# Kernel optimization log

Measured on AMD Instinct MI355X. Metric: run time of the kernel, lower is better.

Reference implementation:

```python
import jax, jax.numpy as jnp
import numpy as np

N_NODES = 100000
N_EDGES = 1600000
IN_CH = 48
OUT_CH = 64
K = 2


def setup_inputs() -> dict:
    key = jax.random.key(0)
    k1, k2, k3, k4 = jax.random.split(key, 4)
    x = jax.random.normal(k1, (N_NODES, IN_CH), dtype=jnp.float32)
    edge_index = jax.random.randint(k2, (2, N_EDGES), 0, N_NODES, dtype=jnp.int64)
    W = jax.random.normal(k3, (IN_CH, OUT_CH), dtype=jnp.float32) * (1.0 / np.sqrt(IN_CH))
    b = jax.random.normal(k4, (OUT_CH,), dtype=jnp.float32) * 0.01
    return {"x": x, "edge_index": edge_index, "W": W, "b": b}


def _propagate(x, row, col):
    n = x.shape[0]
    # degree of each node counted over col (destination) indices
    deg = jax.ops.segment_sum(jnp.ones_like(col, dtype=x.dtype), col, num_segments=n)
    deg_inv_sqrt = jnp.where(deg > 0, jax.lax.rsqrt(jnp.where(deg > 0, deg, 1.0)), 0.0)
    norm = deg_inv_sqrt[row] * deg_inv_sqrt[col]  # [E]
    # gather-scale-scatter: out[col] += x[row] * norm
    msgs = x[row] * norm[:, None]  # [E, d]
    return jax.ops.segment_sum(msgs, col, num_segments=n)


def reference(x, edge_index, W, b):
    row, col = edge_index[0], edge_index[1]
    h = x
    for _ in range(K):
        h = _propagate(h, row, col)
    return h @ W + b
```

## Files before the change

kernel.cpp:

```cpp
#include <hip/hip_runtime.h>
#include <hip/hip_bf16.h>
#include <hip/hip_fp16.h>


#define N_NODES 100000
#define N_EDGES 1600000
#define IN_CH 48
#define OUT_CH 64
#define NBINS 64
#define NBUCKETS 1024
#define EPB 8192
#define NBLK_EDGE 196

__global__ void bucket_hist_kernel(const int* __restrict__ col, int* __restrict__ bucketCount) {
    __shared__ int lh[NBUCKETS];
    for (int i = threadIdx.x; i < NBUCKETS; i += 256) lh[i] = 0;
    __syncthreads();
    int base = blockIdx.x * EPB;
    #pragma unroll 4
    for (int k = 0; k < 32; k++) {
        int e = base + k * 256 + threadIdx.x;
        if (e < N_EDGES) atomicAdd(&lh[col[e] >> 7], 1);
    }
    __syncthreads();
    for (int i = threadIdx.x; i < NBUCKETS; i += 256)
        if (lh[i]) atomicAdd(&bucketCount[i], lh[i]);
}

__global__ void bucket_scan_kernel(const int* __restrict__ bucketCount,
                                   int* __restrict__ bucketStart,
                                   int* __restrict__ bucketCursor) {
    __shared__ int l[NBUCKETS + 1];
    for (int i = threadIdx.x; i < NBUCKETS; i += 256) l[i] = bucketCount[i];
    __syncthreads();
    if (threadIdx.x == 0) {
        int t = 0;
        for (int k = 0; k < NBUCKETS; k++) { int c = l[k]; l[k] = t; t += c; }
        l[NBUCKETS] = t;
    }
    __syncthreads();
    for (int i = threadIdx.x; i <= NBUCKETS; i += 256) {
        bucketStart[i] = l[i];
        if (i < NBUCKETS) bucketCursor[i] = l[i];
    }
}

__global__ void bucket_scatter_kernel(const int* __restrict__ row, const int* __restrict__ col,
                                      int* __restrict__ bucketCursor, int* __restrict__ bucketed) {
    __shared__ int lh[NBUCKETS];
    __shared__ int lofs[NBUCKETS];
    __shared__ int lbase[NBUCKETS];
    __shared__ int stage[EPB];
    __shared__ unsigned short sbkt[EPB];
    __shared__ int wsum[4];
    int tid = threadIdx.x;
    int base = blockIdx.x * EPB;
    for (int i = tid; i < NBUCKETS; i += 256) lh[i] = 0;
    __syncthreads();
    #pragma unroll 4
    for (int k = 0; k < 32; k++) {
        int e = base + k * 256 + tid;
        if (e < N_EDGES) atomicAdd(&lh[col[e] >> 7], 1);
    }
    __syncthreads();
    int c0 = lh[4 * tid], c1 = lh[4 * tid + 1], c2 = lh[4 * tid + 2], c3 = lh[4 * tid + 3];
    {
        int s = c0 + c1 + c2 + c3;
        int incl = s;
        int lane = tid & 63, w = tid >> 6;
        #pragma unroll
        for (int o = 1; o < 64; o <<= 1) {
            int v = __shfl_up(incl, o, 64);
            if (lane >= o) incl += v;
        }
        if (lane == 63) wsum[w] = incl;
        __syncthreads();
        int wbase = 0;
        for (int k = 0; k < w; k++) wbase += wsum[k];
        int ex = wbase + incl - s;
        lofs[4 * tid]     = ex;
        lofs[4 * tid + 1] = ex + c0;
        lofs[4 * tid + 2] = ex + c0 + c1;
        lofs[4 * tid + 3] = ex + c0 + c1 + c2;
    }
    __syncthreads();
    for (int i = tid; i < NBUCKETS; i += 256) {
        int c = lh[i];
        if (c > 0) lbase[i] = atomicAdd(&bucketCursor[i], c);
        lh[i] = 0;
    }
    __syncthreads();
    #pragma unroll 4
    for (int k = 0; k < 32; k++) {
        int e = base + k * 256 + tid;
        if (e < N_EDGES) {
            int c = col[e];
            int bkt = c >> 7;
            int r = atomicAdd(&lh[bkt], 1);
            int slot = lofs[bkt] + r;
            stage[slot] = (row[e] << 7) | (c & 127);
            sbkt[slot] = (unsigned short)bkt;
        }
    }
    __syncthreads();
    int total = (base + EPB <= N_EDGES) ? EPB : (N_EDGES - base);
    for (int i = tid; i < total; i += 256) {
        int bkt = sbkt[i];
        bucketed[lbase[bkt] + (i - lofs[bkt])] = stage[i];
    }
}

__global__ void fine_sort_kernel(const int* __restrict__ bucketed,
                                 const int* __restrict__ bucketStart,
                                 int* __restrict__ edge_src,
                                 int* __restrict__ deg, int* __restrict__ start,
                                 float* __restrict__ dis, int* __restrict__ binTotal) {
    __shared__ int fh[128];
    __shared__ int sfh[129];
    __shared__ int cur[128];
    __shared__ int bh[NBINS];
    int b = blockIdx.x;
    int s0 = bucketStart[b], s1 = bucketStart[b + 1];
    if (threadIdx.x < 128) fh[threadIdx.x] = 0;
    if (threadIdx.x < NBINS) bh[threadIdx.x] = 0;
    __syncthreads();
    for (int j = s0 + threadIdx.x; j < s1; j += 256)
        atomicAdd(&fh[bucketed[j] & 127], 1);
    __syncthreads();
    if (threadIdx.x == 0) {
        int t = 0;
        for (int k = 0; k < 128; k++) { sfh[k] = t; t += fh[k]; }
        sfh[128] = t;
    }
    __syncthreads();
    if (threadIdx.x < 128) {
        cur[threadIdx.x] = sfh[threadIdx.x];
        int node = b * 128 + threadIdx.x;
        if (node < N_NODES) {
            int d = fh[threadIdx.x];
            deg[node] = d;
            start[node] = s0 + sfh[threadIdx.x];
            dis[node] = (d > 0) ? rsqrtf((float)d) : 0.0f;
            atomicAdd(&bh[min(d, NBINS - 1)], 1);
        }
    }
    __syncthreads();
    for (int j = s0 + threadIdx.x; j < s1; j += 256) {
        int rc = bucketed[j];
        int p = atomicAdd(&cur[rc & 127], 1);
        edge_src[s0 + p] = rc >> 7;
    }
    __syncthreads();
    if (threadIdx.x < NBINS && bh[threadIdx.x])
        atomicAdd(&binTotal[threadIdx.x], bh[threadIdx.x]);
}

__global__ void binscan_kernel(const int* __restrict__ binTotal, int* __restrict__ binCursor) {
    if (threadIdx.x == 0) {
        int t = 0;
        for (int k = NBINS - 1; k >= 0; k--) { binCursor[k] = t; t += binTotal[k]; }
    }
}

__global__ void order_kernel(const int* __restrict__ deg, const int* __restrict__ start,
                             const float* __restrict__ dis, int* __restrict__ binCursor,
                             int4* __restrict__ nodeinfo, int n) {
    __shared__ int lhist[NBINS];
    __shared__ int lbase[NBINS];
    int i = blockIdx.x * 256 + threadIdx.x;
    if (threadIdx.x < NBINS) lhist[threadIdx.x] = 0;
    __syncthreads();
    int bin = 0, myrank = 0;
    if (i < n) {
        bin = min(deg[i], NBINS - 1);
        myrank = atomicAdd(&lhist[bin], 1);
    }
    __syncthreads();
    if (threadIdx.x < NBINS && lhist[threadIdx.x] > 0)
        lbase[threadIdx.x] = atomicAdd(&binCursor[threadIdx.x], lhist[threadIdx.x]);
    __syncthreads();
    if (i < n) {
        int pos = lbase[bin] + myrank;
        nodeinfo[pos] = make_int4(i, start[i], deg[i], __float_as_int(dis[i]));
    }
}

__global__ void prescale_kernel(const float* __restrict__ x, const float* __restrict__ dis,
                                __half2* __restrict__ xs, int n2) {
    int i = blockIdx.x * 256 + threadIdx.x;
    if (i < n2) {
        int node = i / 24;
        float2 v = ((const float2*)x)[i];
        float d = dis[node];
        xs[i] = __floats2half2_rn(v.x * d, v.y * d);
    }
}

#define LOAD3(p, v0, v1, v2) { v0 = (p)[0]; v1 = (p)[1]; v2 = (p)[2]; }
#define ACC6(v0, v1, v2) { \
    float2 u0 = __half22float2(v0), u1 = __half22float2(v1), u2 = __half22float2(v2); \
    a0 += u0.x; a1 += u0.y; a2 += u1.x; a3 += u1.y; a4 += u2.x; a5 += u2.y; }

__global__ void gather1_kernel(const __half2* __restrict__ xs,
                               const int* __restrict__ edge_src,
                               const int4* __restrict__ nodeinfo,
                               __half2* __restrict__ h1) {
    int g = blockIdx.x * 32 + (threadIdx.x >> 3);
    int lane = threadIdx.x & 7;
    int4 ni = nodeinfo[g];
    int node = ni.x, s = ni.y, e = ni.y + ni.z;
    float dv = __int_as_float(ni.w);
    float a0 = 0, a1 = 0, a2 = 0, a3 = 0, a4 = 0, a5 = 0;
    int j = s;
    for (; j + 3 < e; j += 4) {
        int s0 = edge_src[j], s1 = edge_src[j + 1], s2 = edge_src[j + 2], s3 = edge_src[j + 3];
        const __half2* p0 = xs + s0 * 24 + lane * 3;
        const __half2* p1 = xs + s1 * 24 + lane * 3;
        const __half2* p2 = xs + s2 * 24 + lane * 3;
        const __half2* p3 = xs + s3 * 24 + lane * 3;
        __half2 v00, v01, v02, v10, v11, v12, v20, v21, v22, v30, v31, v32;
        LOAD3(p0, v00, v01, v02);
        LOAD3(p1, v10, v11, v12);
        LOAD3(p2, v20, v21, v22);
        LOAD3(p3, v30, v31, v32);
        ACC6(v00, v01, v02);
        ACC6(v10, v11, v12);
        ACC6(v20, v21, v22);
        ACC6(v30, v31, v32);
    }
    for (; j < e; ++j) {
        const __half2* p0 = xs + edge_src[j] * 24 + lane * 3;
        __half2 v00, v01, v02;
        LOAD3(p0, v00, v01, v02);
        ACC6(v00, v01, v02);
    }
    float sc = dv * dv;
    __half2* q = h1 + node * 24 + lane * 3;
    q[0] = __floats2half2_rn(a0 * sc, a1 * sc);
    q[1] = __floats2half2_rn(a2 * sc, a3 * sc);
    q[2] = __floats2half2_rn(a4 * sc, a5 * sc);
}

__global__ void gather2_gemm_kernel(const __half2* __restrict__ h1,
                                    const int* __restrict__ edge_src,
                                    const int4* __restrict__ nodeinfo,
                                    const float* __restrict__ W,
                                    const float* __restrict__ b,
                                    float* __restrict__ out) {
    __shared__ float sW[IN_CH * OUT_CH];
    __shared__ float sb[OUT_CH];
    __shared__ float sh[32][IN_CH + 1];

    for (int i = threadIdx.x; i < IN_CH * OUT_CH; i += 256) sW[i] = W[i];
    if (threadIdx.x < OUT_CH) sb[threadIdx.x] = b[threadIdx.x];

    int nl = threadIdx.x >> 3;
    int lane = threadIdx.x & 7;
    int g = blockIdx.x * 32 + nl;
    int4 ni = nodeinfo[g];
    int node = ni.x, s = ni.y, e = ni.y + ni.z;
    float dv = __int_as_float(ni.w);

    float a0 = 0, a1 = 0, a2 = 0, a3 = 0, a4 = 0, a5 = 0;
    int j = s;
    for (; j + 3 < e; j += 4) {
        int s0 = edge_src[j], s1 = edge_src[j + 1], s2 = edge_src[j + 2], s3 = edge_src[j + 3];
        const __half2* p0 = h1 + s0 * 24 + lane * 3;
        const __half2* p1 = h1 + s1 * 24 + lane * 3;
        const __half2* p2 = h1 + s2 * 24 + lane * 3;
        const __half2* p3 = h1 + s3 * 24 + lane * 3;
        __half2 v00, v01, v02, v10, v11, v12, v20, v21, v22, v30, v31, v32;
        LOAD3(p0, v00, v01, v02);
        LOAD3(p1, v10, v11, v12);
        LOAD3(p2, v20, v21, v22);
        LOAD3(p3, v30, v31, v32);
        ACC6(v00, v01, v02);
        ACC6(v10, v11, v12);
        ACC6(v20, v21, v22);
        ACC6(v30, v31, v32);
    }
    for (; j < e; ++j) {
        const __half2* p0 = h1 + edge_src[j] * 24 + lane * 3;
        __half2 v00, v01, v02;
        LOAD3(p0, v00, v01, v02);
        ACC6(v00, v01, v02);
    }
    int c0 = 6 * lane;
    sh[nl][c0 + 0] = a0 * dv;
    sh[nl][c0 + 1] = a1 * dv;
    sh[nl][c0 + 2] = a2 * dv;
    sh[nl][c0 + 3] = a3 * dv;
    sh[nl][c0 + 4] = a4 * dv;
    sh[nl][c0 + 5] = a5 * dv;
    __syncthreads();

    int j0 = lane * 8;
    float acc[8];
    #pragma unroll
    for (int i = 0; i < 8; i++) acc[i] = sb[j0 + i];
    for (int k = 0; k < IN_CH; k++) {
        float s0 = sh[nl][k];
        #pragma unroll
        for (int i = 0; i < 8; i++) acc[i] += s0 * sW[k * OUT_CH + j0 + i];
    }
    float4* o = (float4*)(out + (size_t)node * OUT_CH + j0);
    o[0] = make_float4(acc[0], acc[1], acc[2], acc[3]);
    o[1] = make_float4(acc[4], acc[5], acc[6], acc[7]);
}

extern "C" void kernel_launch(void* const* d_in, const int* in_sizes, int n_in,
                              void* d_out, int out_size, void* d_ws, size_t ws_size,
                              hipStream_t stream) {
    const float* x   = (const float*)d_in[0];
    const int*   ei  = (const int*)d_in[1];
    const float* W   = (const float*)d_in[2];
    const float* b   = (const float*)d_in[3];
    float* out = (float*)d_out;

    const int* row = ei;
    const int* col = ei + N_EDGES;

    int* ws_i = (int*)d_ws;
    int* bucketCount  = ws_i;
    int* binTotal     = ws_i + 1024;
    int* binCursor    = ws_i + 1088;
    int* bucketStart  = ws_i + 1152;
    int* bucketCursor = ws_i + 2304;
    int* deg          = ws_i + 3584;
    int* start        = ws_i + 103936;
    float* dis        = (float*)(ws_i + 204288);
    int4* nodeinfo    = (int4*)(ws_i + 304640);
    int* edge_src     = ws_i + 706048;
    int* bucketed     = ws_i + 2306048;
    __half2* xs       = (__half2*)(ws_i + 2306048);
    __half2* h1       = (__half2*)(ws_i + 4706048);

    hipMemsetAsync(bucketCount, 0, 1088 * sizeof(int), stream);

    bucket_hist_kernel<<<NBLK_EDGE, 256, 0, stream>>>(col, bucketCount);
    bucket_scan_kernel<<<1, 256, 0, stream>>>(bucketCount, bucketStart, bucketCursor);
    bucket_scatter_kernel<<<NBLK_EDGE, 256, 0, stream>>>(row, col, bucketCursor, bucketed);
    fine_sort_kernel<<<(N_NODES + 127) / 128, 256, 0, stream>>>(bucketed, bucketStart,
                                                                edge_src, deg, start, dis, binTotal);
    binscan_kernel<<<1, 64, 0, stream>>>(binTotal, binCursor);
    order_kernel<<<(N_NODES + 255) / 256, 256, 0, stream>>>(deg, start, dis, binCursor,
                                                            nodeinfo, N_NODES);
    prescale_kernel<<<(N_NODES * 24 + 255) / 256, 256, 0, stream>>>(x, dis, xs, N_NODES * 24);

    gather1_kernel<<<N_NODES / 32, 256, 0, stream>>>(xs, edge_src, nodeinfo, h1);
    gather2_gemm_kernel<<<N_NODES / 32, 256, 0, stream>>>(h1, edge_src, nodeinfo, W, b, out);
}
```

Before: 249.1 us.

## Fuse degree ordering and prescale into fine sort with 256-node buckets

Widens coarse buckets to 256 nodes and folds the degree computation, a per-bucket degree-sorted node ordering, and the x prescale into the fine-sort kernel. This removes the binscan, order and prescale launches and the intermediate deg/start/dis arrays. Node ordering becomes local to each 256-node block instead of global by degree, which may reduce load balance in the gather kernels. The gather loops also gain an 8-wide unrolled path with two accumulator sets to expose more memory-level parallelism.

```diff
diff --git a/kernel.cpp b/kernel.cpp
--- a/kernel.cpp
+++ b/kernel.cpp
@@ -7,10 +7,10 @@
 #define N_EDGES 1600000
 #define IN_CH 48
 #define OUT_CH 64
-#define NBINS 64
-#define NBUCKETS 1024
+#define NBUCKETS 392
 #define EPB 8192
 #define NBLK_EDGE 196
+#define NBLK_BKT 391
 
 __global__ void bucket_hist_kernel(const int* __restrict__ col, int* __restrict__ bucketCount) {
     __shared__ int lh[NBUCKETS];
@@ -20,7 +20,7 @@
     #pragma unroll 4
     for (int k = 0; k < 32; k++) {
         int e = base + k * 256 + threadIdx.x;
-        if (e < N_EDGES) atomicAdd(&lh[col[e] >> 7], 1);
+        if (e < N_EDGES) atomicAdd(&lh[col[e] >> 8], 1);
     }
     __syncthreads();
     for (int i = threadIdx.x; i < NBUCKETS; i += 256)
@@ -60,12 +60,13 @@
     #pragma unroll 4
     for (int k = 0; k < 32; k++) {
         int e = base + k * 256 + tid;
-        if (e < N_EDGES) atomicAdd(&lh[col[e] >> 7], 1);
-    }
-    __syncthreads();
-    int c0 = lh[4 * tid], c1 = lh[4 * tid + 1], c2 = lh[4 * tid + 2], c3 = lh[4 * tid + 3];
+        if (e < N_EDGES) atomicAdd(&lh[col[e] >> 8], 1);
+    }
+    __syncthreads();
     {
-        int s = c0 + c1 + c2 + c3;
+        int c0 = (tid < 196) ? lh[2 * tid] : 0;
+        int c1 = (tid < 196) ? lh[2 * tid + 1] : 0;
+        int s = c0 + c1;
         int incl = s;
         int lane = tid & 63, w = tid >> 6;
         #pragma unroll
@@ -78,10 +79,10 @@
         int wbase = 0;
         for (int k = 0; k < w; k++) wbase += wsum[k];
         int ex = wbase + incl - s;
-        lofs[4 * tid]     = ex;
-        lofs[4 * tid + 1] = ex + c0;
-        lofs[4 * tid + 2] = ex + c0 + c1;
-        lofs[4 * tid + 3] = ex + c0 + c1 + c2;
+        if (tid < 196) {
+            lofs[2 * tid]     = ex;
+            lofs[2 * tid + 1] = ex + c0;
+        }
     }
     __syncthreads();
     for (int i = tid; i < NBUCKETS; i += 256) {
@@ -95,10 +96,10 @@
         int e = base + k * 256 + tid;
         if (e < N_EDGES) {
             int c = col[e];
-            int bkt = c >> 7;
+            int bkt = c >> 8;
             int r = atomicAdd(&lh[bkt], 1);
             int slot = lofs[bkt] + r;
-            stage[slot] = (row[e] << 7) | (c & 127);
+            stage[slot] = (row[e] << 8) | (c & 255);
             sbkt[slot] = (unsigned short)bkt;
         }
     }
@@ -112,87 +113,68 @@
 
 __global__ void fine_sort_kernel(const int* __restrict__ bucketed,
                                  const int* __restrict__ bucketStart,
+                                 const float* __restrict__ x,
                                  int* __restrict__ edge_src,
-                                 int* __restrict__ deg, int* __restrict__ start,
-                                 float* __restrict__ dis, int* __restrict__ binTotal) {
-    __shared__ int fh[128];
-    __shared__ int sfh[129];
-    __shared__ int cur[128];
-    __shared__ int bh[NBINS];
+                                 int4* __restrict__ nodeinfo,
+                                 __half2* __restrict__ xs) {
+    __shared__ int fh[256];
+    __shared__ int sfh[257];
+    __shared__ int cur[256];
+    __shared__ int dh[64];
+    __shared__ int dbase[64];
+    __shared__ float fdis[256];
     int b = blockIdx.x;
+    int t = threadIdx.x;
     int s0 = bucketStart[b], s1 = bucketStart[b + 1];
-    if (threadIdx.x < 128) fh[threadIdx.x] = 0;
-    if (threadIdx.x < NBINS) bh[threadIdx.x] = 0;
-    __syncthreads();
-    for (int j = s0 + threadIdx.x; j < s1; j += 256)
-        atomicAdd(&fh[bucketed[j] & 127], 1);
-    __syncthreads();
-    if (threadIdx.x == 0) {
-        int t = 0;
-        for (int k = 0; k < 128; k++) { sfh[k] = t; t += fh[k]; }
-        sfh[128] = t;
-    }
-    __syncthreads();
-    if (threadIdx.x < 128) {
-        cur[threadIdx.x] = sfh[threadIdx.x];
-        int node = b * 128 + threadIdx.x;
-        if (node < N_NODES) {
-            int d = fh[threadIdx.x];
-            deg[node] = d;
-            start[node] = s0 + sfh[threadIdx.x];
-            dis[node] = (d > 0) ? rsqrtf((float)d) : 0.0f;
-            atomicAdd(&bh[min(d, NBINS - 1)], 1);
+    int nodeBase = b << 8;
+    fh[t] = 0;
+    if (t < 64) dh[t] = 0;
+    __syncthreads();
+    for (int j = s0 + t; j < s1; j += 256)
+        atomicAdd(&fh[bucketed[j] & 255], 1);
+    __syncthreads();
+    if (t == 0) {
+        int s = 0;
+        for (int k = 0; k < 256; k++) { sfh[k] = s; s += fh[k]; }
+        sfh[256] = s;
+    }
+    __syncthreads();
+    int node = nodeBase + t;
+    bool valid = (node < N_NODES);
+    int d = fh[t];
+    float dv = (valid && d > 0) ? rsqrtf((float)d) : 0.0f;
+    cur[t] = sfh[t];
+    fdis[t] = dv;
+    int bin = 0, myrank = 0;
+    if (valid) {
+        bin = min(d, 63);
+        myrank = atomicAdd(&dh[bin], 1);
+    }
+    __syncthreads();
+    if (t == 0) {
+        int s = 0;
+        for (int k = 63; k >= 0; k--) { dbase[k] = s; s += dh[k]; }
+    }
+    __syncthreads();
+    if (valid) {
+        int pos = dbase[bin] + myrank;
+        nodeinfo[nodeBase + pos] = make_int4(node, s0 + sfh[t], d, __float_as_int(dv));
+    }
+    for (int i = t; i < 256 * 24; i += 256) {
+        int ln = i / 24;
+        int nd = nodeBase + ln;
+        if (nd < N_NODES) {
+            int ci = i - ln * 24;
+            float dd = fdis[ln];
+            float2 v = ((const float2*)x)[nd * 24 + ci];
+            xs[nd * 24 + ci] = __floats2half2_rn(v.x * dd, v.y * dd);
         }
     }
     __syncthreads();
-    for (int j = s0 + threadIdx.x; j < s1; j += 256) {
+    for (int j = s0 + t; j < s1; j += 256) {
         int rc = bucketed[j];
-        int p = atomicAdd(&cur[rc & 127], 1);
-        edge_src[s0 + p] = rc >> 7;
-    }
-    __syncthreads();
-    if (threadIdx.x < NBINS && bh[threadIdx.x])
-        atomicAdd(&binTotal[threadIdx.x], bh[threadIdx.x]);
-}
-
-__global__ void binscan_kernel(const int* __restrict__ binTotal, int* __restrict__ binCursor) {
-    if (threadIdx.x == 0) {
-        int t = 0;
-        for (int k = NBINS - 1; k >= 0; k--) { binCursor[k] = t; t += binTotal[k]; }
-    }
-}
-
-__global__ void order_kernel(const int* __restrict__ deg, const int* __restrict__ start,
-                             const float* __restrict__ dis, int* __restrict__ binCursor,
-                             int4* __restrict__ nodeinfo, int n) {
-    __shared__ int lhist[NBINS];
-    __shared__ int lbase[NBINS];
-    int i = blockIdx.x * 256 + threadIdx.x;
-    if (threadIdx.x < NBINS) lhist[threadIdx.x] = 0;
-    __syncthreads();
-    int bin = 0, myrank = 0;
-    if (i < n) {
-        bin = min(deg[i], NBINS - 1);
-        myrank = atomicAdd(&lhist[bin], 1);
-    }
-    __syncthreads();
-    if (threadIdx.x < NBINS && lhist[threadIdx.x] > 0)
-        lbase[threadIdx.x] = atomicAdd(&binCursor[threadIdx.x], lhist[threadIdx.x]);
-    __syncthreads();
-    if (i < n) {
-        int pos = lbase[bin] + myrank;
-        nodeinfo[pos] = make_int4(i, start[i], deg[i], __float_as_int(dis[i]));
-    }
-}
-
-__global__ void prescale_kernel(const float* __restrict__ x, const float* __restrict__ dis,
-                                __half2* __restrict__ xs, int n2) {
-    int i = blockIdx.x * 256 + threadIdx.x;
-    if (i < n2) {
-        int node = i / 24;
-        float2 v = ((const float2*)x)[i];
-        float d = dis[node];
-        xs[i] = __floats2half2_rn(v.x * d, v.y * d);
+        int p = atomicAdd(&cur[rc & 255], 1);
+        edge_src[s0 + p] = rc >> 8;
     }
 }
 
@@ -200,6 +182,9 @@
 #define ACC6(v0, v1, v2) { \
     float2 u0 = __half22float2(v0), u1 = __half22float2(v1), u2 = __half22float2(v2); \
     a0 += u0.x; a1 += u0.y; a2 += u1.x; a3 += u1.y; a4 += u2.x; a5 += u2.y; }
+#define ACC6B(v0, v1, v2) { \
+    float2 u0 = __half22float2(v0), u1 = __half22float2(v1), u2 = __half22float2(v2); \
+    b0 += u0.x; b1 += u0.y; b2 += u1.x; b3 += u1.y; b4 += u2.x; b5 += u2.y; }
 
 __global__ void gather1_kernel(const __half2* __restrict__ xs,
                                const int* __restrict__ edge_src,
@@ -211,22 +196,41 @@
     int node = ni.x, s = ni.y, e = ni.y + ni.z;
     float dv = __int_as_float(ni.w);
     float a0 = 0, a1 = 0, a2 = 0, a3 = 0, a4 = 0, a5 = 0;
+    float b0 = 0, b1 = 0, b2 = 0, b3 = 0, b4 = 0, b5 = 0;
     int j = s;
+    for (; j + 7 < e; j += 8) {
+        int s0 = edge_src[j],     s1 = edge_src[j + 1], s2 = edge_src[j + 2], s3 = edge_src[j + 3];
+        int s4 = edge_src[j + 4], s5 = edge_src[j + 5], s6 = edge_src[j + 6], s7 = edge_src[j + 7];
+        const __half2* p0 = xs + s0 * 24 + lane * 3;
+        const __half2* p1 = xs + s1 * 24 + lane * 3;
+        const __half2* p2 = xs + s2 * 24 + lane * 3;
+        const __half2* p3 = xs + s3 * 24 + lane * 3;
+        const __half2* p4 = xs + s4 * 24 + lane * 3;
+        const __half2* p5 = xs + s5 * 24 + lane * 3;
+        const __half2* p6 = xs + s6 * 24 + lane * 3;
+        const __half2* p7 = xs + s7 * 24 + lane * 3;
+        __half2 v00,v01,v02, v10,v11,v12, v20,v21,v22, v30,v31,v32;
+        __half2 v40,v41,v42, v50,v51,v52, v60,v61,v62, v70,v71,v72;
+        LOAD3(p0, v00, v01, v02); LOAD3(p1, v10, v11, v12);
+        LOAD3(p2, v20, v21, v22); LOAD3(p3, v30, v31, v32);
+        LOAD3(p4, v40, v41, v42); LOAD3(p5, v50, v51, v52);
+        LOAD3(p6, v60, v61, v62); LOAD3(p7, v70, v71, v72);
+        ACC6(v00, v01, v02); ACC6B(v10, v11, v12);
+        ACC6(v20, v21, v22); ACC6B(v30, v31, v32);
+        ACC6(v40, v41, v42); ACC6B(v50, v51, v52);
+        ACC6(v60, v61, v62); ACC6B(v70, v71, v72);
+    }
     for (; j + 3 < e; j += 4) {
         int s0 = edge_src[j], s1 = edge_src[j + 1], s2 = edge_src[j + 2], s3 = edge_src[j + 3];
         const __half2* p0 = xs + s0 * 24 + lane * 3;
         const __half2* p1 = xs + s1 * 24 + lane * 3;
         const __half2* p2 = xs + s2 * 24 + lane * 3;
         const __half2* p3 = xs + s3 * 24 + lane * 3;
-        __half2 v00, v01, v02, v10, v11, v12, v20, v21, v22, v30, v31, v32;
-        LOAD3(p0, v00, v01, v02);
-        LOAD3(p1, v10, v11, v12);
-        LOAD3(p2, v20, v21, v22);
-        LOAD3(p3, v30, v31, v32);
-        ACC6(v00, v01, v02);
-        ACC6(v10, v11, v12);
-        ACC6(v20, v21, v22);
-        ACC6(v30, v31, v32);
+        __half2 v00,v01,v02, v10,v11,v12, v20,v21,v22, v30,v31,v32;
+        LOAD3(p0, v00, v01, v02); LOAD3(p1, v10, v11, v12);
+        LOAD3(p2, v20, v21, v22); LOAD3(p3, v30, v31, v32);
+        ACC6(v00, v01, v02); ACC6B(v10, v11, v12);
+        ACC6(v20, v21, v22); ACC6B(v30, v31, v32);
     }
     for (; j < e; ++j) {
         const __half2* p0 = xs + edge_src[j] * 24 + lane * 3;
@@ -234,6 +238,7 @@
         LOAD3(p0, v00, v01, v02);
         ACC6(v00, v01, v02);
     }
+    a0 += b0; a1 += b1; a2 += b2; a3 += b3; a4 += b4; a5 += b5;
     float sc = dv * dv;
     __half2* q = h1 + node * 24 + lane * 3;
     q[0] = __floats2half2_rn(a0 * sc, a1 * sc);
@@ -245,14 +250,14 @@
                                     const int* __restrict__ edge_src,
                                     const int4* __restrict__ nodeinfo,
                                     const float* __restrict__ W,
-                                    const float* __restrict__ b,
+                                    const float* __restrict__ bias,
                                     float* __restrict__ out) {
     __shared__ float sW[IN_CH * OUT_CH];
     __shared__ float sb[OUT_CH];
     __shared__ float sh[32][IN_CH + 1];
 
     for (int i = threadIdx.x; i < IN_CH * OUT_CH; i += 256) sW[i] = W[i];
-    if (threadIdx.x < OUT_CH) sb[threadIdx.x] = b[threadIdx.x];
+    if (threadIdx.x < OUT_CH) sb[threadIdx.x] = bias[threadIdx.x];
 
     int nl = threadIdx.x >> 3;
     int lane = threadIdx.x & 7;
@@ -262,22 +267,41 @@
     float dv = __int_as_float(ni.w);
 
     float a0 = 0, a1 = 0, a2 = 0, a3 = 0, a4 = 0, a5 = 0;
+    float b0 = 0, b1 = 0, b2 = 0, b3 = 0, b4 = 0, b5 = 0;
     int j = s;
+    for (; j + 7 < e; j += 8) {
+        int s0 = edge_src[j],     s1 = edge_src[j + 1], s2 = edge_src[j + 2], s3 = edge_src[j + 3];
+        int s4 = edge_src[j + 4], s5 = edge_src[j + 5], s6 = edge_src[j + 6], s7 = edge_src[j + 7];
+        const __half2* p0 = h1 + s0 * 24 + lane * 3;
+        const __half2* p1 = h1 + s1 * 24 + lane * 3;
+        const __half2* p2 = h1 + s2 * 24 + lane * 3;
+        const __half2* p3 = h1 + s3 * 24 + lane * 3;
+        const __half2* p4 = h1 + s4 * 24 + lane * 3;
+        const __half2* p5 = h1 + s5 * 24 + lane * 3;
+        const __half2* p6 = h1 + s6 * 24 + lane * 3;
+        const __half2* p7 = h1 + s7 * 24 + lane * 3;
+        __half2 v00,v01,v02, v10,v11,v12, v20,v21,v22, v30,v31,v32;
+        __half2 v40,v41,v42, v50,v51,v52, v60,v61,v62, v70,v71,v72;
+        LOAD3(p0, v00, v01, v02); LOAD3(p1, v10, v11, v12);
+        LOAD3(p2, v20, v21, v22); LOAD3(p3, v30, v31, v32);
+        LOAD3(p4, v40, v41, v42); LOAD3(p5, v50, v51, v52);
+        LOAD3(p6, v60, v61, v62); LOAD3(p7, v70, v71, v72);
+        ACC6(v00, v01, v02); ACC6B(v10, v11, v12);
+        ACC6(v20, v21, v22); ACC6B(v30, v31, v32);
+        ACC6(v40, v41, v42); ACC6B(v50, v51, v52);
+        ACC6(v60, v61, v62); ACC6B(v70, v71, v72);
+    }
     for (; j + 3 < e; j += 4) {
         int s0 = edge_src[j], s1 = edge_src[j + 1], s2 = edge_src[j + 2], s3 = edge_src[j + 3];
         const __half2* p0 = h1 + s0 * 24 + lane * 3;
         const __half2* p1 = h1 + s1 * 24 + lane * 3;
         const __half2* p2 = h1 + s2 * 24 + lane * 3;
         const __half2* p3 = h1 + s3 * 24 + lane * 3;
-        __half2 v00, v01, v02, v10, v11, v12, v20, v21, v22, v30, v31, v32;
-        LOAD3(p0, v00, v01, v02);
-        LOAD3(p1, v10, v11, v12);
-        LOAD3(p2, v20, v21, v22);
-        LOAD3(p3, v30, v31, v32);
-        ACC6(v00, v01, v02);
-        ACC6(v10, v11, v12);
-        ACC6(v20, v21, v22);
-        ACC6(v30, v31, v32);
+        __half2 v00,v01,v02, v10,v11,v12, v20,v21,v22, v30,v31,v32;
+        LOAD3(p0, v00, v01, v02); LOAD3(p1, v10, v11, v12);
+        LOAD3(p2, v20, v21, v22); LOAD3(p3, v30, v31, v32);
+        ACC6(v00, v01, v02); ACC6B(v10, v11, v12);
+        ACC6(v20, v21, v22); ACC6B(v30, v31, v32);
     }
     for (; j < e; ++j) {
         const __half2* p0 = h1 + edge_src[j] * 24 + lane * 3;
@@ -285,6 +309,7 @@
         LOAD3(p0, v00, v01, v02);
         ACC6(v00, v01, v02);
     }
+    a0 += b0; a1 += b1; a2 += b2; a3 += b3; a4 += b4; a5 += b5;
     int c0 = 6 * lane;
     sh[nl][c0 + 0] = a0 * dv;
     sh[nl][c0 + 1] = a1 * dv;
@@ -322,30 +347,21 @@
 
     int* ws_i = (int*)d_ws;
     int* bucketCount  = ws_i;
-    int* binTotal     = ws_i + 1024;
-    int* binCursor    = ws_i + 1088;
-    int* bucketStart  = ws_i + 1152;
-    int* bucketCursor = ws_i + 2304;
-    int* deg          = ws_i + 3584;
-    int* start        = ws_i + 103936;
-    float* dis        = (float*)(ws_i + 204288);
-    int4* nodeinfo    = (int4*)(ws_i + 304640);
-    int* edge_src     = ws_i + 706048;
-    int* bucketed     = ws_i + 2306048;
-    __half2* xs       = (__half2*)(ws_i + 2306048);
-    __half2* h1       = (__half2*)(ws_i + 4706048);
-
-    hipMemsetAsync(bucketCount, 0, 1088 * sizeof(int), stream);
+    int* bucketStart  = ws_i + 512;
+    int* bucketCursor = ws_i + 1024;
+    int4* nodeinfo    = (int4*)(ws_i + 2048);
+    int* edge_src     = ws_i + 403456;
+    int* bucketed     = ws_i + 2003456;
+    __half2* xs       = (__half2*)(ws_i + 3603456);
+    __half2* h1       = (__half2*)(ws_i + 6003456);
+
+    hipMemsetAsync(bucketCount, 0, NBUCKETS * sizeof(int), stream);
 
     bucket_hist_kernel<<<NBLK_EDGE, 256, 0, stream>>>(col, bucketCount);
     bucket_scan_kernel<<<1, 256, 0, stream>>>(bucketCount, bucketStart, bucketCursor);
     bucket_scatter_kernel<<<NBLK_EDGE, 256, 0, stream>>>(row, col, bucketCursor, bucketed);
-    fine_sort_kernel<<<(N_NODES + 127) / 128, 256, 0, stream>>>(bucketed, bucketStart,
-                                                                edge_src, deg, start, dis, binTotal);
-    binscan_kernel<<<1, 64, 0, stream>>>(binTotal, binCursor);
-    order_kernel<<<(N_NODES + 255) / 256, 256, 0, stream>>>(deg, start, dis, binCursor,
-                                                            nodeinfo, N_NODES);
-    prescale_kernel<<<(N_NODES * 24 + 255) / 256, 256, 0, stream>>>(x, dis, xs, N_NODES * 24);
+    fine_sort_kernel<<<NBLK_BKT, 256, 0, stream>>>(bucketed, bucketStart, x,
+                                                   edge_src, nodeinfo, xs);
 
     gather1_kernel<<<N_NODES / 32, 256, 0, stream>>>(xs, edge_src, nodeinfo, h1);
     gather2_gemm_kernel<<<N_NODES / 32, 256, 0, stream>>>(h1, edge_src, nodeinfo, W, b, out);
```

Result: no change. 251.5 us (+1.0%).
